# Optimization experiments

Measured on AMD Instinct MI355X. Metric: run time of the kernel, lower is better.

Reference implementation:

```python
import jax, jax.numpy as jnp
import numpy as np

B, T, H = 8, 1024, 640
N_PHONE, N_PHONEME = 230, 96


def _make_mapping():
    # 0/1 phone->phoneme allophone map, shape (n_phoneme, n_phone).
    # Every phone maps to >=1 phoneme; every phoneme covered (n_phone > n_phoneme).
    rng = np.random.default_rng(0)
    m = np.zeros((N_PHONEME, N_PHONE), dtype=np.float32)
    cols = np.arange(N_PHONE)
    m[cols % N_PHONEME, cols] = 1.0
    m[rng.integers(0, N_PHONEME, size=N_PHONE), cols] = 1.0  # some phones are allophones of 2 phonemes
    m[0, 0] = 1.0  # blank -> blank, as in allophone_layer
    return jnp.asarray(m)


def setup_inputs() -> dict:
    key = jax.random.key(0)
    k1, k2 = jax.random.split(key)
    enc_output = jax.random.normal(k1, (B, T, H), dtype=jnp.float32)
    feature2phone = jax.random.normal(k2, (H, N_PHONE), dtype=jnp.float32)
    return {"enc_output": enc_output, "feature2phone": feature2phone, "mapping": _make_mapping()}


def reference(enc_output, feature2phone, mapping):
    # phone logits: (B,T,H) @ (H,P) -> (B,T,P), scaled by sqrt(H)
    hidden = feature2phone.shape[0]
    phone = jnp.einsum('bth,hp->btp', enc_output, feature2phone) / jnp.sqrt(jnp.asarray(hidden, enc_output.dtype))
    # broadcast-multiply with 0/1 map -> (B,T,M,P), mask zeros with -inf
    allo = phone[:, :, None, :] * mapping  # mapping: (M,P)
    allo = jnp.where(mapping > 0, allo, -jnp.inf)
    # masked max segment-reduce over the phone axis -> (B,T,M)
    phoneme = jnp.max(allo, axis=-1)
    # log-softmax over phoneme dim
    return jax.nn.log_softmax(phoneme, axis=2)
```

## Files before the change

### kernel.cpp

```cpp
#include <hip/hip_runtime.h>
#include <math.h>

#define NH 640
#define NP 230
#define NM 96
#define NROWS 8192
#define MAXL 32
#define NSTEP 20
#define NRT 512

#define OFF_CNT  0
#define OFF_CSR  4096
#define OFF_B    65536

typedef __bf16 bf16_t;
typedef bf16_t bf16x8 __attribute__((ext_vector_type(8)));
typedef float floatx4 __attribute__((ext_vector_type(4)));

static __device__ __forceinline__ unsigned short f2b(float f) {
    unsigned u = __float_as_uint(f);
    u += 0x7fffu + ((u >> 16) & 1u);
    return (unsigned short)(u >> 16);
}

__global__ __launch_bounds__(256)
void prep_kernel(const float* __restrict__ f2p,
                 const float* __restrict__ mapping,
                 int* __restrict__ cnt, int* __restrict__ csr,
                 unsigned short* __restrict__ wsB2) {
    const int b = blockIdx.x;
    const int tid = threadIdx.x;
    if (b < 24) {
        int wave = b * 4 + (tid >> 6);
        int lane = tid & 63;
        if (wave >= NM) return;
        int base = 0;
        #pragma unroll
        for (int c = 0; c < 4; ++c) {
            int p = c * 64 + lane;
            float v = (p < NP) ? mapping[wave * NP + p] : 0.0f;
            unsigned long long mask = __ballot(v > 0.0f);
            if (v > 0.0f) {
                int idx = base + __popcll(mask & ((1ull << lane) - 1ull));
                if (idx < MAXL) csr[wave * MAXL + idx] = p;
            }
            base += __popcll(mask);
        }
        if (lane == 0) cnt[wave] = base < MAXL ? base : MAXL;
    } else {
        int g = (b - 24) * 256 + tid;
        int m16  = g & 15;
        int quad = (g >> 4) & 3;
        int ct   = (g >> 6) & 15;
        int s    = g >> 10;
        int n = ct * 16 + m16;
        int k0 = s * 32 + quad * 8;
        unsigned short v[8];
        #pragma unroll
        for (int j = 0; j < 8; ++j)
            v[j] = (n < NP) ? f2b(f2p[(size_t)(k0 + j) * NP + n]) : (unsigned short)0;
        *(uint4*)(wsB2 + (size_t)g * 8) = *(const uint4*)v;
    }
}

__global__ __launch_bounds__(256, 2)
void fused_phonetics_kernel(const float* __restrict__ enc,
                            const unsigned short* __restrict__ wsB2,
                            const int* __restrict__ cnt,
                            const int* __restrict__ csr,
                            float* __restrict__ out) {
    __shared__ float phone[16][257];

    const int tid  = threadIdx.x;
    const int lane = tid & 63;
    const int wv   = tid >> 6;
    const int m16  = lane & 15;
    const int quad = lane >> 4;
    const int rt   = blockIdx.x;
    const int row0 = rt * 16;

    floatx4 acc0 = {0.f,0.f,0.f,0.f}, acc1 = acc0, acc2 = acc0, acc3 = acc0;

    const float* arow = enc + (size_t)(row0 + m16) * NH + quad * 8;
    const unsigned short* bptr = wsB2 + ((size_t)(wv * 4) * 64 + lane) * 8;

    #pragma unroll
    for (int s = 0; s < NSTEP; ++s) {
        float4 a0 = *(const float4*)(arow + s * 32);
        float4 a1 = *(const float4*)(arow + s * 32 + 4);
        uint4 b0 = *(const uint4*)(bptr + ((size_t)s * 16 + 0) * 64 * 8);
        uint4 b1 = *(const uint4*)(bptr + ((size_t)s * 16 + 1) * 64 * 8);
        uint4 b2 = *(const uint4*)(bptr + ((size_t)s * 16 + 2) * 64 * 8);
        uint4 b3 = *(const uint4*)(bptr + ((size_t)s * 16 + 3) * 64 * 8);
        union { unsigned short s16[8]; bf16x8 v; } au;
        au.s16[0] = f2b(a0.x); au.s16[1] = f2b(a0.y);
        au.s16[2] = f2b(a0.z); au.s16[3] = f2b(a0.w);
        au.s16[4] = f2b(a1.x); au.s16[5] = f2b(a1.y);
        au.s16[6] = f2b(a1.z); au.s16[7] = f2b(a1.w);
        bf16x8 af = au.v;
        acc0 = __builtin_amdgcn_mfma_f32_16x16x32_bf16(af, __builtin_bit_cast(bf16x8, b0), acc0, 0, 0, 0);
        acc1 = __builtin_amdgcn_mfma_f32_16x16x32_bf16(af, __builtin_bit_cast(bf16x8, b1), acc1, 0, 0, 0);
        acc2 = __builtin_amdgcn_mfma_f32_16x16x32_bf16(af, __builtin_bit_cast(bf16x8, b2), acc2, 0, 0, 0);
        acc3 = __builtin_amdgcn_mfma_f32_16x16x32_bf16(af, __builtin_bit_cast(bf16x8, b3), acc3, 0, 0, 0);
    }

    const float scale = 0.03952847075210474f;
    #pragma unroll
    for (int i = 0; i < 4; ++i) {
        int r = quad * 4 + i;
        phone[r][wv * 64 +  0 + m16] = acc0[i] * scale;
        phone[r][wv * 64 + 16 + m16] = acc1[i] * scale;
        phone[r][wv * 64 + 32 + m16] = acc2[i] * scale;
        phone[r][wv * 64 + 48 + m16] = acc3[i] * scale;
    }
    __syncthreads();

    const int r   = tid >> 4;
    const int l16 = tid & 15;
    float pmv[6];
    float mx = -INFINITY;
    #pragma unroll
    for (int j = 0; j < 6; ++j) {
        int m = l16 + j * 16;
        int c = cnt[m];
        const int* lst = csr + m * MAXL;
        float best = -INFINITY;
        for (int jj = 0; jj < c; ++jj) best = fmaxf(best, phone[r][lst[jj]]);
        pmv[j] = best;
        mx = fmaxf(mx, best);
    }
    #pragma unroll
    for (int d = 1; d < 16; d <<= 1) mx = fmaxf(mx, __shfl_xor(mx, d));
    float s = 0.f;
    #pragma unroll
    for (int j = 0; j < 6; ++j) s += __expf(pmv[j] - mx);
    #pragma unroll
    for (int d = 1; d < 16; d <<= 1) s += __shfl_xor(s, d);
    const float lse = mx + __logf(s);
    #pragma unroll
    for (int j = 0; j < 6; ++j)
        out[(size_t)(row0 + r) * NM + l16 + j * 16] = pmv[j] - lse;
}

extern "C" void kernel_launch(void* const* d_in, const int* in_sizes, int n_in,
                              void* d_out, int out_size, void* d_ws, size_t ws_size,
                              hipStream_t stream) {
    const float* enc     = (const float*)d_in[0];
    const float* f2p     = (const float*)d_in[1];
    const float* mapping = (const float*)d_in[2];
    float* out = (float*)d_out;

    char* ws = (char*)d_ws;
    int* cnt = (int*)(ws + OFF_CNT);
    int* csr = (int*)(ws + OFF_CSR);
    unsigned short* wsB2 = (unsigned short*)(ws + OFF_B);

    prep_kernel<<<104, 256, 0, stream>>>(f2p, mapping, cnt, csr, wsB2);
    fused_phonetics_kernel<<<NRT, 256, 0, stream>>>(enc, wsB2, cnt, csr, out);
}
```

Measured before the change: 91.63 us.

## Stage bf16 A tile in shared memory and share B across 32-row blocks

Each block now covers 32 rows with 512 threads. It first loads the encoder rows with coalesced float4 reads, converts them to bf16 once and stores them in shared memory in MFMA fragment order. Eight waves split the work into two row halves and four column quarters, so each B fragment load from global memory serves two row tiles. The phone buffer reuses the same shared memory after a barrier. This halves the grid size and adds a serialized staging phase before the MFMA loop.

```diff
diff --git a/kernel.cpp b/kernel.cpp
--- a/kernel.cpp
+++ b/kernel.cpp
@@ -7,7 +7,8 @@
 #define NROWS 8192
 #define MAXL 32
 #define NSTEP 20
-#define NRT 512
+#define MBLK 32
+#define NBLOCKS (NROWS / MBLK)
 
 #define OFF_CNT  0
 #define OFF_CSR  4096
@@ -63,55 +64,69 @@
     }
 }
 
-__global__ __launch_bounds__(256, 2)
+__global__ __launch_bounds__(512, 1)
 void fused_phonetics_kernel(const float* __restrict__ enc,
                             const unsigned short* __restrict__ wsB2,
                             const int* __restrict__ cnt,
                             const int* __restrict__ csr,
                             float* __restrict__ out) {
-    __shared__ float phone[16][257];
+    __shared__ __align__(16) unsigned short sA[2560 * 8];
+    float (*phone)[257] = (float (*)[257])sA;
 
     const int tid  = threadIdx.x;
     const int lane = tid & 63;
     const int wv   = tid >> 6;
     const int m16  = lane & 15;
     const int quad = lane >> 4;
-    const int rt   = blockIdx.x;
-    const int row0 = rt * 16;
+    const int rh   = wv & 1;
+    const int cq   = wv >> 1;
+    const int row0 = blockIdx.x * MBLK;
+
+    #pragma unroll
+    for (int i = 0; i < 10; ++i) {
+        int F = i * 2048 + tid * 4;
+        int row = F / 640;
+        int k   = F - row * 640;
+        float4 a = *(const float4*)(enc + (size_t)row0 * NH + F);
+        int s  = k >> 5;
+        int q  = (k & 31) >> 3;
+        int j0 = k & 7;
+        unsigned short v[4];
+        v[0] = f2b(a.x); v[1] = f2b(a.y); v[2] = f2b(a.z); v[3] = f2b(a.w);
+        int soff = ((s * 2 + (row >> 4)) * 64 + q * 16 + (row & 15)) * 8 + j0;
+        *(uint2*)(sA + soff) = *(const uint2*)v;
+    }
+    __syncthreads();
 
     floatx4 acc0 = {0.f,0.f,0.f,0.f}, acc1 = acc0, acc2 = acc0, acc3 = acc0;
 
-    const float* arow = enc + (size_t)(row0 + m16) * NH + quad * 8;
-    const unsigned short* bptr = wsB2 + ((size_t)(wv * 4) * 64 + lane) * 8;
+    const unsigned short* aptr = sA + ((size_t)rh * 64 + lane) * 8;
+    const unsigned short* bptr = wsB2 + ((size_t)(cq * 4) * 64 + lane) * 8;
 
     #pragma unroll
     for (int s = 0; s < NSTEP; ++s) {
-        float4 a0 = *(const float4*)(arow + s * 32);
-        float4 a1 = *(const float4*)(arow + s * 32 + 4);
+        uint4 a  = *(const uint4*)(aptr + (size_t)(s * 2) * 64 * 8);
         uint4 b0 = *(const uint4*)(bptr + ((size_t)s * 16 + 0) * 64 * 8);
         uint4 b1 = *(const uint4*)(bptr + ((size_t)s * 16 + 1) * 64 * 8);
         uint4 b2 = *(const uint4*)(bptr + ((size_t)s * 16 + 2) * 64 * 8);
         uint4 b3 = *(const uint4*)(bptr + ((size_t)s * 16 + 3) * 64 * 8);
-        union { unsigned short s16[8]; bf16x8 v; } au;
-        au.s16[0] = f2b(a0.x); au.s16[1] = f2b(a0.y);
-        au.s16[2] = f2b(a0.z); au.s16[3] = f2b(a0.w);
-        au.s16[4] = f2b(a1.x); au.s16[5] = f2b(a1.y);
-        au.s16[6] = f2b(a1.z); au.s16[7] = f2b(a1.w);
-        bf16x8 af = au.v;
+        bf16x8 af = __builtin_bit_cast(bf16x8, a);
         acc0 = __builtin_amdgcn_mfma_f32_16x16x32_bf16(af, __builtin_bit_cast(bf16x8, b0), acc0, 0, 0, 0);
         acc1 = __builtin_amdgcn_mfma_f32_16x16x32_bf16(af, __builtin_bit_cast(bf16x8, b1), acc1, 0, 0, 0);
         acc2 = __builtin_amdgcn_mfma_f32_16x16x32_bf16(af, __builtin_bit_cast(bf16x8, b2), acc2, 0, 0, 0);
         acc3 = __builtin_amdgcn_mfma_f32_16x16x32_bf16(af, __builtin_bit_cast(bf16x8, b3), acc3, 0, 0, 0);
     }
 
+    __syncthreads();
+
     const float scale = 0.03952847075210474f;
     #pragma unroll
     for (int i = 0; i < 4; ++i) {
-        int r = quad * 4 + i;
-        phone[r][wv * 64 +  0 + m16] = acc0[i] * scale;
-        phone[r][wv * 64 + 16 + m16] = acc1[i] * scale;
-        phone[r][wv * 64 + 32 + m16] = acc2[i] * scale;
-        phone[r][wv * 64 + 48 + m16] = acc3[i] * scale;
+        int r = rh * 16 + quad * 4 + i;
+        phone[r][cq * 64 +  0 + m16] = acc0[i] * scale;
+        phone[r][cq * 64 + 16 + m16] = acc1[i] * scale;
+        phone[r][cq * 64 + 32 + m16] = acc2[i] * scale;
+        phone[r][cq * 64 + 48 + m16] = acc3[i] * scale;
     }
     __syncthreads();
 
@@ -156,5 +171,5 @@
     unsigned short* wsB2 = (unsigned short*)(ws + OFF_B);
 
     prep_kernel<<<104, 256, 0, stream>>>(f2p, mapping, cnt, csr, wsB2);
-    fused_phonetics_kernel<<<NRT, 256, 0, stream>>>(enc, wsB2, cnt, csr, out);
+    fused_phonetics_kernel<<<NBLOCKS, 512, 0, stream>>>(enc, wsB2, cnt, csr, out);
 }
```

Measured after the change: 87.55 us. 1.05x faster.
